# Optimization experiments

Hardware: AMD Instinct MI355X
Metric: run time of the kernel (lower is better)

Reference implementation:

```python
import jax, jax.numpy as jnp
import numpy as np

HIDDEN = 512
QK_DIM = HIDDEN // 8  # 64
B, H, W = 32, 32, 32


def conv1x1(x, w, b):
    # 1x1 conv == channel matmul: w [out_c, in_c], x [b, in_c, h, w]
    return jnp.einsum('oc,bchw->bohw', w, x) + b[None, :, None, None]


def setup_inputs() -> dict:
    key = jax.random.key(0)
    ks = jax.random.split(key, 10)
    s = 0.02
    return {
        'x': jax.random.normal(ks[0], (B, HIDDEN, H, W), jnp.float32),
        'pos_embedding': jax.random.normal(ks[1], (1, HIDDEN, 32, 32), jnp.float32),
        'query_w': jax.random.normal(ks[2], (QK_DIM, HIDDEN), jnp.float32) * s,
        'query_b': jax.random.normal(ks[3], (QK_DIM,), jnp.float32) * s,
        'key_w': jax.random.normal(ks[4], (QK_DIM, HIDDEN), jnp.float32) * s,
        'key_b': jax.random.normal(ks[5], (QK_DIM,), jnp.float32) * s,
        'value_w': jax.random.normal(ks[6], (HIDDEN, HIDDEN), jnp.float32) * s,
        'value_b': jax.random.normal(ks[7], (HIDDEN,), jnp.float32) * s,
        'out_w': jax.random.normal(ks[8], (HIDDEN, HIDDEN), jnp.float32) * s,
        'out_b': jax.random.normal(ks[9], (HIDDEN,), jnp.float32) * s,
    }


def reference(x, pos_embedding, query_w, query_b, key_w, key_b,
              value_w, value_b, out_w, out_b):
    b, c, h, w = x.shape
    n = h * w
    x = x + pos_embedding[:, :, :h, :w]
    q = conv1x1(x, query_w, query_b).reshape(b, -1, n)   # [b, d, n]
    k = conv1x1(x, key_w, key_b).reshape(b, -1, n)       # [b, d, n]
    v = conv1x1(x, value_w, value_b).reshape(b, -1, n)   # [b, c, n]
    # scores[b,i,j] = sum_d q[b,d,i] * k[b,d,j]  (no 1/sqrt(d) scaling, faithful)
    scores = jnp.einsum('bdi,bdj->bij', q, k)
    attn = jax.nn.softmax(scores, axis=-1)               # [b, n, n]
    # out[b,c,i] = sum_j v[b,c,j] * attn[b,i,j]
    out = jnp.einsum('bcj,bij->bci', v, attn).reshape(b, c, h, w)
    return conv1x1(out, out_w, out_b)
```

## Files before the change

kernel.cpp:

```cpp
#include <hip/hip_runtime.h>

#define BB 32
#define CC 512
#define DD 64
#define NN 1024
#define GRP 16
#define NGRP (BB / GRP)

typedef float4 f4;
typedef __attribute__((ext_vector_type(8))) short bf16x8;
typedef __attribute__((ext_vector_type(4))) float f32x4;
typedef __attribute__((ext_vector_type(4))) unsigned short us4;
typedef __attribute__((ext_vector_type(8))) unsigned short us8;

__device__ inline unsigned short bf16rn(float f) {
  union { float f; unsigned u; } v; v.f = f;
  unsigned r = v.u + 0x7fff + ((v.u >> 16) & 1);
  return (unsigned short)(r >> 16);
}

__device__ inline void gl_lds16(const void* g, void* l) {
  __builtin_amdgcn_global_load_lds(
      (const __attribute__((address_space(1))) unsigned int*)g,
      (__attribute__((address_space(3))) unsigned int*)l, 16, 0, 0);
}

__device__ inline void wait_vm0_barrier() {
  asm volatile("s_waitcnt vmcnt(0)" ::: "memory");
  __builtin_amdgcn_s_barrier();
}

__device__ inline int xcd_swz(int bid, int nwg) {
  return (bid & 7) * (nwg >> 3) + (bid >> 3);
}

template <int KDIM>
__device__ inline void gemm_core(const unsigned short* __restrict__ A,
                                 const unsigned short* __restrict__ Bt,
                                 int m0, int n0, int tid,
                                 unsigned short* sA, unsigned short* sB,
                                 f32x4 acc[4][4]) {
  const int wave = tid >> 6, lane = tid & 63;
  const int wm = (wave & 1) * 64, wn = (wave >> 1) * 64;
  const int fm = lane & 15;
  const int kq = lane >> 4;
  const int srow = lane >> 3;
  const int sg   = (lane & 7) ^ srow;

  const unsigned short* ga = A  + (size_t)(m0 + srow) * KDIM + sg * 8;
  const unsigned short* gb = Bt + (size_t)(n0 + srow) * KDIM + sg * 8;

  auto stage = [&](int buf, int k0) {
#pragma unroll
    for (int t = 0; t < 4; ++t) {
      const int R = wave * 32 + t * 8;
      gl_lds16(ga + (size_t)R * KDIM + k0, sA + buf * 8192 + R * 64);
      gl_lds16(gb + (size_t)R * KDIM + k0, sB + buf * 8192 + R * 64);
    }
  };

  stage(0, 0);
  wait_vm0_barrier();

  int cur = 0;
  for (int k0 = 0; k0 < KDIM; k0 += 64) {
    if (k0 + 64 < KDIM) stage(cur ^ 1, k0 + 64);
    const unsigned short* pA = sA + cur * 8192;
    const unsigned short* pB = sB + cur * 8192;
#pragma unroll
    for (int ks = 0; ks < 2; ++ks) {
      bf16x8 af[4], bfr[4];
#pragma unroll
      for (int i = 0; i < 4; ++i) {
        const int ra = wm + i * 16 + fm;
        const int rb = wn + i * 16 + fm;
        af[i]  = *(const bf16x8*)(pA + ra * 64 + ((ks * 4 + kq) ^ (ra & 7)) * 8);
        bfr[i] = *(const bf16x8*)(pB + rb * 64 + ((ks * 4 + kq) ^ (rb & 7)) * 8);
      }
#pragma unroll
      for (int i = 0; i < 4; ++i)
#pragma unroll
        for (int j = 0; j < 4; ++j)
          acc[i][j] = __builtin_amdgcn_mfma_f32_16x16x32_bf16(af[i], bfr[j], acc[i][j], 0, 0, 0);
    }
    wait_vm0_barrier();
    cur ^= 1;
  }
}

__global__ __launch_bounds__(256) void prep_w(
    const float* __restrict__ qw, const float* __restrict__ kw, const float* __restrict__ vw,
    const float* __restrict__ qb, const float* __restrict__ kb, const float* __restrict__ vb,
    const float* __restrict__ ow,
    unsigned short* __restrict__ wcat, unsigned short* __restrict__ owb,
    float* __restrict__ bcat) {
  int idx = blockIdx.x * 256 + threadIdx.x;
  if (idx < 640 * 512) {
    int row = idx >> 9;
    float v = (row < 64) ? qw[idx] : (row < 128) ? kw[idx - 64 * 512] : vw[idx - 128 * 512];
    wcat[idx] = bf16rn(v);
    if (idx < 640) bcat[idx] = (idx < 64) ? qb[idx] : (idx < 128) ? kb[idx - 64] : vb[idx - 128];
  } else {
    int j = idx - 640 * 512;
    owb[j] = bf16rn(ow[j]);
  }
}

__global__ __launch_bounds__(256) void prep_x(const float* __restrict__ x,
                                              const float* __restrict__ pos,
                                              unsigned short* __restrict__ A) {
  __shared__ float t[64][65];
  const int b = blockIdx.z, i0 = blockIdx.x * 64, c0 = blockIdx.y * 64;
  const int tid = threadIdx.x;
  const int ci = tid >> 4, il = (tid & 15) * 4;
  const float* xb = x + (size_t)b * CC * NN;
#pragma unroll
  for (int r = 0; r < 4; ++r) {
    int cl = r * 16 + ci;
    f4 xv = *(const f4*)(xb  + (size_t)(c0 + cl) * NN + i0 + il);
    f4 pv = *(const f4*)(pos + (size_t)(c0 + cl) * NN + i0 + il);
    t[cl][il + 0] = xv.x + pv.x;
    t[cl][il + 1] = xv.y + pv.y;
    t[cl][il + 2] = xv.z + pv.z;
    t[cl][il + 3] = xv.w + pv.w;
  }
  __syncthreads();
  const int iw = tid >> 2, cw = (tid & 3) * 16;
  unsigned short* dst = A + ((size_t)b * NN + i0 + iw) * CC + c0 + cw;
  us8 p0, p1;
#pragma unroll
  for (int j = 0; j < 8; ++j) p0[j] = bf16rn(t[cw + j][iw]);
#pragma unroll
  for (int j = 0; j < 8; ++j) p1[j] = bf16rn(t[cw + 8 + j][iw]);
  *(us8*)dst = p0;
  *(us8*)(dst + 8) = p1;
}

__global__ __launch_bounds__(256) void proj_gemm(
    const unsigned short* __restrict__ A, const unsigned short* __restrict__ wcat,
    const float* __restrict__ bcat,
    unsigned short* __restrict__ qo, unsigned short* __restrict__ ko,
    unsigned short* __restrict__ vto) {
  __shared__ unsigned short sA[16384], sB[16384];
  const int wid = xcd_swz(blockIdx.x, 1280);
  const int m0 = (wid & 7) * 128, n0 = ((wid >> 3) % 5) * 128, b = wid / 40;
  const int tid = threadIdx.x, wave = tid >> 6, lane = tid & 63;
  f32x4 acc[4][4];
#pragma unroll
  for (int i = 0; i < 4; ++i)
#pragma unroll
    for (int j = 0; j < 4; ++j) acc[i][j] = (f32x4)(0.0f);

  gemm_core<512>(A + (size_t)b * NN * CC, wcat, m0, n0, tid, sA, sB, acc);

  const int wm = (wave & 1) * 64, wn = (wave >> 1) * 64;
#pragma unroll
  for (int i = 0; i < 4; ++i)
#pragma unroll
    for (int j = 0; j < 4; ++j) {
      int col  = n0 + wn + j * 16 + (lane & 15);
      int rowb = m0 + wm + i * 16 + (lane >> 4) * 4;
      float bias = bcat[col];
      if (col < 64) {
#pragma unroll
        for (int r = 0; r < 4; ++r)
          qo[((size_t)b * NN + rowb + r) * DD + col] = bf16rn(acc[i][j][r] + bias);
      } else if (col < 128) {
#pragma unroll
        for (int r = 0; r < 4; ++r)
          ko[((size_t)b * NN + rowb + r) * DD + col - 64] = bf16rn(acc[i][j][r] + bias);
      } else {
        int c = col - 128;
        us4 pk;
#pragma unroll
        for (int r = 0; r < 4; ++r) pk[r] = bf16rn(acc[i][j][r] + bias);
        *(us4*)(vto + ((size_t)b * CC + c) * NN + rowb) = pk;
      }
    }
}

__global__ __launch_bounds__(256) void qkexp_kernel(
    const unsigned short* __restrict__ q, const unsigned short* __restrict__ k,
    float* __restrict__ lpart, unsigned short* __restrict__ P) {
  __shared__ unsigned short sQ[8192];
  __shared__ unsigned short sK[16384];
  __shared__ float wred[4][128];

  const int wid = xcd_swz(blockIdx.x, 8 * 2 * GRP);
  const int i0 = (wid & 7) * 128, jc = (wid >> 3) & 1, b = wid >> 4;
  const int jbase = jc * 512;
  const int tid = threadIdx.x, wave = tid >> 6, lane = tid & 63;
  const int wm = (wave & 1) * 64, wn = (wave >> 1) * 64;
  const int fm = lane & 15, kq = lane >> 4;
  const int srow = lane >> 3, sg = (lane & 7) ^ srow;

  const unsigned short* qb = q + (size_t)b * NN * DD;
  const unsigned short* kb = k + (size_t)b * NN * DD;

  auto stageK = [&](int buf, int j0) {
#pragma unroll
    for (int t = 0; t < 4; ++t) {
      const int R = wave * 32 + t * 8;
      gl_lds16(kb + (size_t)(j0 + R + srow) * DD + sg * 8, sK + buf * 8192 + R * 64);
    }
  };

#pragma unroll
  for (int t = 0; t < 4; ++t) {
    const int R = wave * 32 + t * 8;
    gl_lds16(qb + (size_t)(i0 + R + srow) * DD + sg * 8, sQ + R * 64);
  }
  stageK(0, jbase);
  wait_vm0_barrier();

  bf16x8 aq[4][2];
#pragma unroll
  for (int i = 0; i < 4; ++i)
#pragma unroll
    for (int kd = 0; kd < 2; ++kd) {
      const int ra = wm + i * 16 + fm;
      aq[i][kd] = *(const bf16x8*)(sQ + ra * 64 + ((kd * 4 + kq) ^ (ra & 7)) * 8);
    }

  float l_l[4] = {0.f, 0.f, 0.f, 0.f};

  int cur = 0;
#pragma unroll
  for (int jt = 0; jt < 4; ++jt) {
    if (jt < 3) stageK(cur ^ 1, jbase + (jt + 1) * 128);
    const unsigned short* pK = sK + cur * 8192;
    f32x4 S[4][4];
#pragma unroll
    for (int jk = 0; jk < 4; ++jk)
#pragma unroll
      for (int iq = 0; iq < 4; ++iq) S[jk][iq] = (f32x4)(0.0f);
#pragma unroll
    for (int kd = 0; kd < 2; ++kd) {
      bf16x8 bk[4];
#pragma unroll
      for (int jk = 0; jk < 4; ++jk) {
        const int rb = wn + jk * 16 + fm;
        bk[jk] = *(const bf16x8*)(pK + rb * 64 + ((kd * 4 + kq) ^ (rb & 7)) * 8);
      }
#pragma unroll
      for (int jk = 0; jk < 4; ++jk)
#pragma unroll
        for (int iq = 0; iq < 4; ++iq)
          S[jk][iq] = __builtin_amdgcn_mfma_f32_16x16x32_bf16(bk[jk], aq[iq][kd], S[jk][iq], 0, 0, 0);
    }
    us4 pk[4][4];
#pragma unroll
    for (int jk = 0; jk < 4; ++jk)
#pragma unroll
      for (int iq = 0; iq < 4; ++iq) {
#pragma unroll
        for (int r = 0; r < 4; ++r) {
          float e = __expf(S[jk][iq][r]);
          pk[jk][iq][r] = bf16rn(e);
          l_l[iq] += e;
        }
      }
    wait_vm0_barrier();
#pragma unroll
    for (int jk = 0; jk < 4; ++jk)
#pragma unroll
      for (int iq = 0; iq < 4; ++iq) {
        const int row = i0 + wm + iq * 16 + fm;
        const int col = jbase + jt * 128 + wn + jk * 16 + kq * 4;
        *(us4*)(P + ((size_t)b * NN + row) * NN + col) = pk[jk][iq];
      }
    cur ^= 1;
  }

#pragma unroll
  for (int iq = 0; iq < 4; ++iq) {
    float l = l_l[iq];
    l += __shfl_xor(l, 16, 64);
    l += __shfl_xor(l, 32, 64);
    l_l[iq] = l;
  }
  if (lane < 16) {
#pragma unroll
    for (int iq = 0; iq < 4; ++iq) wred[wave][wm + iq * 16 + fm] = l_l[iq];
  }
  __syncthreads();
  if (tid < 128) {
    const int a = tid >> 6;
    float l = wred[a][tid] + wred[a + 2][tid];
    lpart[((size_t)b * NN + i0 + tid) * 2 + jc] = l;
  }
}

__global__ __launch_bounds__(256) void pv_gemm(
    const unsigned short* __restrict__ P, const unsigned short* __restrict__ vT,
    const float* __restrict__ lpart, unsigned short* __restrict__ attnout) {
  __shared__ unsigned short sA[16384], sB[16384];
  const int wid = xcd_swz(blockIdx.x, 8 * 4 * GRP);
  const int m0 = (wid & 7) * 128, n0 = ((wid >> 3) & 3) * 128, b = wid >> 5;
  const int tid = threadIdx.x, wave = tid >> 6, lane = tid & 63;
  f32x4 acc[4][4];
#pragma unroll
  for (int i = 0; i < 4; ++i)
#pragma unroll
    for (int j = 0; j < 4; ++j) acc[i][j] = (f32x4)(0.0f);

  gemm_core<1024>(P + (size_t)b * NN * NN, vT + (size_t)b * CC * NN, m0, n0, tid, sA, sB, acc);

  const int wm = (wave & 1) * 64, wn = (wave >> 1) * 64;
  float inv[4][4];
#pragma unroll
  for (int i = 0; i < 4; ++i)
#pragma unroll
    for (int r = 0; r < 4; ++r) {
      const int row = m0 + wm + i * 16 + (lane >> 4) * 4 + r;
      float2 lp = *(const float2*)(lpart + ((size_t)b * NN + row) * 2);
      inv[i][r] = 1.0f / (lp.x + lp.y);
    }
#pragma unroll
  for (int i = 0; i < 4; ++i)
#pragma unroll
    for (int j = 0; j < 4; ++j) {
      int col  = n0 + wn + j * 16 + (lane & 15);
      int rowb = m0 + wm + i * 16 + (lane >> 4) * 4;
#pragma unroll
      for (int r = 0; r < 4; ++r)
        attnout[((size_t)b * NN + rowb + r) * CC + col] = bf16rn(acc[i][j][r] * inv[i][r]);
    }
}

__global__ __launch_bounds__(256) void outproj_gemm(
    const unsigned short* __restrict__ owb, const unsigned short* __restrict__ attnout,
    const float* __restrict__ ob, float* __restrict__ out) {
  __shared__ unsigned short sA[16384], sB[16384];
  const int wid = xcd_swz(blockIdx.x, 1024);
  const int m0 = (wid & 3) * 128, n0 = ((wid >> 2) & 7) * 128, b = wid >> 5;
  const int tid = threadIdx.x, wave = tid >> 6, lane = tid & 63;
  f32x4 acc[4][4];
#pragma unroll
  for (int i = 0; i < 4; ++i)
#pragma unroll
    for (int j = 0; j < 4; ++j) acc[i][j] = (f32x4)(0.0f);

  gemm_core<512>(owb, attnout + (size_t)b * NN * CC, m0, n0, tid, sA, sB, acc);

  const int wm = (wave & 1) * 64, wn = (wave >> 1) * 64;
#pragma unroll
  for (int i = 0; i < 4; ++i)
#pragma unroll
    for (int j = 0; j < 4; ++j) {
      int col  = n0 + wn + j * 16 + (lane & 15);
      int rowb = m0 + wm + i * 16 + (lane >> 4) * 4;
      f4 b4 = *(const f4*)(ob + rowb);
#pragma unroll
      for (int r = 0; r < 4; ++r)
        out[((size_t)b * CC + rowb + r) * NN + col] = acc[i][j][r] + ((const float*)&b4)[r];
    }
}

extern "C" void kernel_launch(void* const* d_in, const int* in_sizes, int n_in,
                              void* d_out, int out_size, void* d_ws, size_t ws_size,
                              hipStream_t stream) {
  const float* x   = (const float*)d_in[0];
  const float* pos = (const float*)d_in[1];
  const float* qw  = (const float*)d_in[2];
  const float* qb  = (const float*)d_in[3];
  const float* kw  = (const float*)d_in[4];
  const float* kb  = (const float*)d_in[5];
  const float* vw  = (const float*)d_in[6];
  const float* vb  = (const float*)d_in[7];
  const float* ow  = (const float*)d_in[8];
  const float* ob  = (const float*)d_in[9];
  float* out = (float*)d_out;

  char* w = (char*)d_ws;
  unsigned short* wcat = (unsigned short*)w; w += (size_t)640 * 512 * 2;
  unsigned short* owb  = (unsigned short*)w; w += (size_t)512 * 512 * 2;
  float*          bcat = (float*)w;          w += 640 * 4;
  unsigned short* A    = (unsigned short*)w; w += (size_t)BB * NN * CC * 2;
  unsigned short* q    = (unsigned short*)w; w += (size_t)BB * NN * DD * 2;
  unsigned short* k    = (unsigned short*)w; w += (size_t)BB * NN * DD * 2;
  unsigned short* vT   = (unsigned short*)w; w += (size_t)BB * CC * NN * 2;
  float*         lpart = (float*)w;          w += (size_t)BB * NN * 2 * 4;
  unsigned short* PG   = (unsigned short*)w; w += (size_t)GRP * NN * NN * 2;
  unsigned short* attnout = A;

  hipLaunchKernelGGL(prep_w, dim3(2304), dim3(256), 0, stream,
                     qw, kw, vw, qb, kb, vb, ow, wcat, owb, bcat);
  hipLaunchKernelGGL(prep_x, dim3(16, 8, 32), dim3(256), 0, stream, x, pos, A);
  hipLaunchKernelGGL(proj_gemm, dim3(1280), dim3(256), 0, stream,
                     A, wcat, bcat, q, k, vT);

  for (int g = 0; g < NGRP; ++g) {
    const unsigned short* qg  = q  + (size_t)g * GRP * NN * DD;
    const unsigned short* kg  = k  + (size_t)g * GRP * NN * DD;
    const unsigned short* vTg = vT + (size_t)g * GRP * CC * NN;
    float*                lpg = lpart + (size_t)g * GRP * NN * 2;
    unsigned short* aog = attnout + (size_t)g * GRP * NN * CC;
    hipLaunchKernelGGL(qkexp_kernel, dim3(8 * 2 * GRP), dim3(256), 0, stream,
                       qg, kg, lpg, PG);
    hipLaunchKernelGGL(pv_gemm, dim3(8 * 4 * GRP), dim3(256), 0, stream,
                       PG, vTg, lpg, aog);
  }

  hipLaunchKernelGGL(outproj_gemm, dim3(1024), dim3(256), 0, stream,
                     owb, attnout, ob, out);
}
```

Baseline: 283.5 us.

## Use triple-buffered BK=32 GEMM pipeline and defer P stores in scores kernel

The shared GEMM core moves from a double-buffered K-step of 64 with a full vmcnt(0) wait and barrier each step to a three-stage ring of 32-wide K tiles. Partial vmcnt waits let two tiles stay in flight, and the LDS footprint per block drops. The scores kernel now issues each P tile's global stores one iteration later, behind the next tile's MFMAs, and uses partial waits instead of draining all memory ops. The risks are finer-grained barriers with fewer MFMAs between them, and vmcnt counts that must exactly match the number of outstanding loads and stores.

After: 303.8 us. 7.2% more time.

```diff
diff --git a/kernel.cpp b/kernel.cpp
--- a/kernel.cpp
+++ b/kernel.cpp
@@ -35,56 +35,61 @@
 }
 
 template <int KDIM>
-__device__ inline void gemm_core(const unsigned short* __restrict__ A,
-                                 const unsigned short* __restrict__ Bt,
-                                 int m0, int n0, int tid,
-                                 unsigned short* sA, unsigned short* sB,
-                                 f32x4 acc[4][4]) {
+__device__ inline void gemm_core32(const unsigned short* __restrict__ A,
+                                   const unsigned short* __restrict__ Bt,
+                                   int m0, int n0, int tid,
+                                   unsigned short* sA, unsigned short* sB,
+                                   f32x4 acc[4][4]) {
+  constexpr int NT = KDIM / 32;
   const int wave = tid >> 6, lane = tid & 63;
   const int wm = (wave & 1) * 64, wn = (wave >> 1) * 64;
   const int fm = lane & 15;
   const int kq = lane >> 4;
-  const int srow = lane >> 3;
-  const int sg   = (lane & 7) ^ srow;
-
-  const unsigned short* ga = A  + (size_t)(m0 + srow) * KDIM + sg * 8;
-  const unsigned short* gb = Bt + (size_t)(n0 + srow) * KDIM + sg * 8;
+  const int srow = lane >> 2;
+  const int sg8  = ((lane & 3) ^ ((lane >> 3) & 3)) * 8;
+  const int slotA = (kq ^ ((fm >> 1) & 3)) * 8;
+
+  const unsigned short* ga = A  + (size_t)(m0 + srow) * KDIM + sg8;
+  const unsigned short* gb = Bt + (size_t)(n0 + srow) * KDIM + sg8;
 
   auto stage = [&](int buf, int k0) {
 #pragma unroll
-    for (int t = 0; t < 4; ++t) {
-      const int R = wave * 32 + t * 8;
-      gl_lds16(ga + (size_t)R * KDIM + k0, sA + buf * 8192 + R * 64);
-      gl_lds16(gb + (size_t)R * KDIM + k0, sB + buf * 8192 + R * 64);
+    for (int t = 0; t < 2; ++t) {
+      const int R0 = wave * 32 + t * 16;
+      gl_lds16(ga + (size_t)R0 * KDIM + k0, sA + buf * 4096 + R0 * 32);
+      gl_lds16(gb + (size_t)R0 * KDIM + k0, sB + buf * 4096 + R0 * 32);
     }
   };
 
   stage(0, 0);
-  wait_vm0_barrier();
+  stage(1, 32);
 
   int cur = 0;
-  for (int k0 = 0; k0 < KDIM; k0 += 64) {
-    if (k0 + 64 < KDIM) stage(cur ^ 1, k0 + 64);
-    const unsigned short* pA = sA + cur * 8192;
-    const unsigned short* pB = sB + cur * 8192;
-#pragma unroll
-    for (int ks = 0; ks < 2; ++ks) {
-      bf16x8 af[4], bfr[4];
-#pragma unroll
-      for (int i = 0; i < 4; ++i) {
-        const int ra = wm + i * 16 + fm;
-        const int rb = wn + i * 16 + fm;
-        af[i]  = *(const bf16x8*)(pA + ra * 64 + ((ks * 4 + kq) ^ (ra & 7)) * 8);
-        bfr[i] = *(const bf16x8*)(pB + rb * 64 + ((ks * 4 + kq) ^ (rb & 7)) * 8);
-      }
-#pragma unroll
-      for (int i = 0; i < 4; ++i)
-#pragma unroll
-        for (int j = 0; j < 4; ++j)
-          acc[i][j] = __builtin_amdgcn_mfma_f32_16x16x32_bf16(af[i], bfr[j], acc[i][j], 0, 0, 0);
-    }
-    wait_vm0_barrier();
-    cur ^= 1;
+  for (int i = 0; i < NT; ++i) {
+    if (i + 1 < NT) {
+      asm volatile("s_waitcnt vmcnt(4)" ::: "memory");
+    } else {
+      asm volatile("s_waitcnt vmcnt(0)" ::: "memory");
+    }
+    __builtin_amdgcn_s_barrier();
+    if (i + 2 < NT) {
+      int nb = cur + 2; if (nb >= 3) nb -= 3;
+      stage(nb, (i + 2) * 32);
+    }
+    const unsigned short* pA = sA + cur * 4096;
+    const unsigned short* pB = sB + cur * 4096;
+    bf16x8 af[4], bfr[4];
+#pragma unroll
+    for (int ii = 0; ii < 4; ++ii) {
+      af[ii]  = *(const bf16x8*)(pA + (wm + ii * 16 + fm) * 32 + slotA);
+      bfr[ii] = *(const bf16x8*)(pB + (wn + ii * 16 + fm) * 32 + slotA);
+    }
+#pragma unroll
+    for (int ii = 0; ii < 4; ++ii)
+#pragma unroll
+      for (int j = 0; j < 4; ++j)
+        acc[ii][j] = __builtin_amdgcn_mfma_f32_16x16x32_bf16(af[ii], bfr[j], acc[ii][j], 0, 0, 0);
+    cur += 1; if (cur >= 3) cur -= 3;
   }
 }
 
@@ -141,7 +146,7 @@
     const float* __restrict__ bcat,
     unsigned short* __restrict__ qo, unsigned short* __restrict__ ko,
     unsigned short* __restrict__ vto) {
-  __shared__ unsigned short sA[16384], sB[16384];
+  __shared__ unsigned short sA[12288], sB[12288];
   const int wid = xcd_swz(blockIdx.x, 1280);
   const int m0 = (wid & 7) * 128, n0 = ((wid >> 3) % 5) * 128, b = wid / 40;
   const int tid = threadIdx.x, wave = tid >> 6, lane = tid & 63;
@@ -151,7 +156,7 @@
 #pragma unroll
     for (int j = 0; j < 4; ++j) acc[i][j] = (f32x4)(0.0f);
 
-  gemm_core<512>(A + (size_t)b * NN * CC, wcat, m0, n0, tid, sA, sB, acc);
+  gemm_core32<512>(A + (size_t)b * NN * CC, wcat, m0, n0, tid, sA, sB, acc);
 
   const int wm = (wave & 1) * 64, wn = (wave >> 1) * 64;
 #pragma unroll
@@ -223,11 +228,23 @@
     }
 
   float l_l[4] = {0.f, 0.f, 0.f, 0.f};
+  us4 pk[4][4];
+  int pjt = 0;
 
   int cur = 0;
 #pragma unroll
   for (int jt = 0; jt < 4; ++jt) {
     if (jt < 3) stageK(cur ^ 1, jbase + (jt + 1) * 128);
+    if (jt > 0) {
+#pragma unroll
+      for (int jk = 0; jk < 4; ++jk)
+#pragma unroll
+        for (int iq = 0; iq < 4; ++iq) {
+          const int row = i0 + wm + iq * 16 + fm;
+          const int col = jbase + pjt * 128 + wn + jk * 16 + kq * 4;
+          *(us4*)(P + ((size_t)b * NN + row) * NN + col) = pk[jk][iq];
+        }
+    }
     const unsigned short* pK = sK + cur * 8192;
     f32x4 S[4][4];
 #pragma unroll
@@ -248,7 +265,6 @@
         for (int iq = 0; iq < 4; ++iq)
           S[jk][iq] = __builtin_amdgcn_mfma_f32_16x16x32_bf16(bk[jk], aq[iq][kd], S[jk][iq], 0, 0, 0);
     }
-    us4 pk[4][4];
 #pragma unroll
     for (int jk = 0; jk < 4; ++jk)
 #pragma unroll
@@ -260,17 +276,22 @@
           l_l[iq] += e;
         }
       }
-    wait_vm0_barrier();
-#pragma unroll
-    for (int jk = 0; jk < 4; ++jk)
-#pragma unroll
-      for (int iq = 0; iq < 4; ++iq) {
-        const int row = i0 + wm + iq * 16 + fm;
-        const int col = jbase + jt * 128 + wn + jk * 16 + kq * 4;
-        *(us4*)(P + ((size_t)b * NN + row) * NN + col) = pk[jk][iq];
-      }
+    pjt = jt;
+    if (jt < 3) {
+      if (jt == 0) { asm volatile("s_waitcnt vmcnt(0)" ::: "memory"); }
+      else         { asm volatile("s_waitcnt vmcnt(16)" ::: "memory"); }
+      __builtin_amdgcn_s_barrier();
+    }
     cur ^= 1;
   }
+#pragma unroll
+  for (int jk = 0; jk < 4; ++jk)
+#pragma unroll
+    for (int iq = 0; iq < 4; ++iq) {
+      const int row = i0 + wm + iq * 16 + fm;
+      const int col = jbase + 3 * 128 + wn + jk * 16 + kq * 4;
+      *(us4*)(P + ((size_t)b * NN + row) * NN + col) = pk[jk][iq];
+    }
 
 #pragma unroll
   for (int iq = 0; iq < 4; ++iq) {
@@ -294,7 +315,7 @@
 __global__ __launch_bounds__(256) void pv_gemm(
     const unsigned short* __restrict__ P, const unsigned short* __restrict__ vT,
     const float* __restrict__ lpart, unsigned short* __restrict__ attnout) {
-  __shared__ unsigned short sA[16384], sB[16384];
+  __shared__ unsigned short sA[12288], sB[12288];
   const int wid = xcd_swz(blockIdx.x, 8 * 4 * GRP);
   const int m0 = (wid & 7) * 128, n0 = ((wid >> 3) & 3) * 128, b = wid >> 5;
   const int tid = threadIdx.x, wave = tid >> 6, lane = tid & 63;
@@ -304,7 +325,7 @@
 #pragma unroll
     for (int j = 0; j < 4; ++j) acc[i][j] = (f32x4)(0.0f);
 
-  gemm_core<1024>(P + (size_t)b * NN * NN, vT + (size_t)b * CC * NN, m0, n0, tid, sA, sB, acc);
+  gemm_core32<1024>(P + (size_t)b * NN * NN, vT + (size_t)b * CC * NN, m0, n0, tid, sA, sB, acc);
 
   const int wm = (wave & 1) * 64, wn = (wave >> 1) * 64;
   float inv[4][4];
@@ -331,7 +352,7 @@
 __global__ __launch_bounds__(256) void outproj_gemm(
     const unsigned short* __restrict__ owb, const unsigned short* __restrict__ attnout,
     const float* __restrict__ ob, float* __restrict__ out) {
-  __shared__ unsigned short sA[16384], sB[16384];
+  __shared__ unsigned short sA[12288], sB[12288];
   const int wid = xcd_swz(blockIdx.x, 1024);
   const int m0 = (wid & 3) * 128, n0 = ((wid >> 2) & 7) * 128, b = wid >> 5;
   const int tid = threadIdx.x, wave = tid >> 6, lane = tid & 63;
@@ -341,7 +362,7 @@
 #pragma unroll
     for (int j = 0; j < 4; ++j) acc[i][j] = (f32x4)(0.0f);
 
-  gemm_core<512>(owb, attnout + (size_t)b * NN * CC, m0, n0, tid, sA, sB, acc);
+  gemm_core32<512>(owb, attnout + (size_t)b * NN * CC, m0, n0, tid, sA, sB, acc);
 
   const int wm = (wave & 1) * 64, wn = (wave >> 1) * 64;
 #pragma unroll
```

## Rewrite output projection GEMM with 256x256 tiles and double-buffered LDS pipeline

Applied to the files above, without the earlier changes.

Replaces the 128x128-tile output projection (1024 blocks of 256 threads) with a 256x256-tile kernel using 8 waves per block (256 blocks of 512 threads). Global-to-LDS loads go into double-buffered, XOR-swizzled shared memory and are staged in pieces interleaved with the MFMA phases, with explicit vmcnt waits and barriers. The aim is more operand reuse per LDS load and overlap of loads with compute. The cost is 128 KB of LDS and a large accumulator per wave, which limits the GPU to one block per CU, and 256 blocks may underfill the device.

New measurement: 288.2 us. Within noise of the previous version (+1.7%).

```diff
diff --git a/kernel.cpp b/kernel.cpp
--- a/kernel.cpp
+++ b/kernel.cpp
@@ -328,32 +328,97 @@
     }
 }
 
-__global__ __launch_bounds__(256) void outproj_gemm(
+__global__ __launch_bounds__(512, 1) void outproj_gemm8(
     const unsigned short* __restrict__ owb, const unsigned short* __restrict__ attnout,
     const float* __restrict__ ob, float* __restrict__ out) {
-  __shared__ unsigned short sA[16384], sB[16384];
-  const int wid = xcd_swz(blockIdx.x, 1024);
-  const int m0 = (wid & 3) * 128, n0 = ((wid >> 2) & 7) * 128, b = wid >> 5;
+  __shared__ unsigned short sA[2][16384];
+  __shared__ unsigned short sB[2][16384];
+
+  const int wid = xcd_swz(blockIdx.x, 256);
+  const int m0 = (wid & 1) * 256, n0 = ((wid >> 1) & 3) * 256, b = wid >> 3;
   const int tid = threadIdx.x, wave = tid >> 6, lane = tid & 63;
-  f32x4 acc[4][4];
-#pragma unroll
-  for (int i = 0; i < 4; ++i)
+  const int wave_m = wave >> 2, wave_n = wave & 3;
+  const int wm = wave_m * 128, wn = wave_n * 64;
+  const int fm = lane & 15, kq = lane >> 4;
+  const int srow = lane >> 3, sg = (lane & 7) ^ srow;
+
+  const unsigned short* ga = owb + (size_t)(m0 + srow) * 512 + sg * 8;
+  const unsigned short* gb = attnout + (size_t)b * NN * CC + (size_t)(n0 + srow) * 512 + sg * 8;
+
+  auto stageB4 = [&](int buf, int k0) {
+#pragma unroll
+    for (int s = 0; s < 4; ++s) {
+      const int R = s * 64 + wave * 8;
+      gl_lds16(gb + (size_t)R * 512 + k0, &sB[buf][R * 64]);
+    }
+  };
+  auto stageA2 = [&](int buf, int k0, int h) {
+#pragma unroll
+    for (int t = 0; t < 2; ++t) {
+      const int R = (h + t * 2) * 64 + wave * 8;
+      gl_lds16(ga + (size_t)R * 512 + k0, &sA[buf][R * 64]);
+    }
+  };
+
+  f32x4 acc[8][4];
+#pragma unroll
+  for (int i = 0; i < 8; ++i)
 #pragma unroll
     for (int j = 0; j < 4; ++j) acc[i][j] = (f32x4)(0.0f);
 
-  gemm_core<512>(owb, attnout + (size_t)b * NN * CC, m0, n0, tid, sA, sB, acc);
-
-  const int wm = (wave & 1) * 64, wn = (wave >> 1) * 64;
-#pragma unroll
-  for (int i = 0; i < 4; ++i)
+  stageB4(0, 0); stageA2(0, 0, 0); stageA2(0, 0, 1);
+
+  for (int t = 0; t < 8; ++t) {
+    const int cur = t & 1;
+    const int k0n = (t + 1) * 64;
+    const unsigned short* pA = sA[cur];
+    const unsigned short* pB = sB[cur];
+
+#pragma unroll
+    for (int p = 0; p < 4; ++p) {
+      const int ih = p >> 1, kw = p & 1;
+      if (p == 0) {
+        asm volatile("s_waitcnt vmcnt(2)" ::: "memory");
+        __builtin_amdgcn_s_barrier();
+        if (t < 7) stageB4(cur ^ 1, k0n);
+      } else if (p == 2) {
+        if (t < 7) { asm volatile("s_waitcnt vmcnt(6)" ::: "memory"); }
+        else       { asm volatile("s_waitcnt vmcnt(0)" ::: "memory"); }
+        __builtin_amdgcn_s_barrier();
+        if (t < 7) stageA2(cur ^ 1, k0n, 1);
+      } else if (p == 1) {
+        if (t < 7) stageA2(cur ^ 1, k0n, 0);
+      }
+      bf16x8 af[4], bfr[4];
+#pragma unroll
+      for (int i = 0; i < 4; ++i) {
+        const int ra = wm + ih * 64 + i * 16 + fm;
+        af[i] = *(const bf16x8*)(pA + ra * 64 + ((kw * 4 + kq) ^ (ra & 7)) * 8);
+      }
+#pragma unroll
+      for (int j = 0; j < 4; ++j) {
+        const int rb = wn + j * 16 + fm;
+        bfr[j] = *(const bf16x8*)(pB + rb * 64 + ((kw * 4 + kq) ^ (rb & 7)) * 8);
+      }
+#pragma unroll
+      for (int i = 0; i < 4; ++i)
+#pragma unroll
+        for (int j = 0; j < 4; ++j)
+          acc[ih * 4 + i][j] =
+              __builtin_amdgcn_mfma_f32_16x16x32_bf16(af[i], bfr[j], acc[ih * 4 + i][j], 0, 0, 0);
+    }
+  }
+
+#pragma unroll
+  for (int ig = 0; ig < 8; ++ig)
 #pragma unroll
     for (int j = 0; j < 4; ++j) {
-      int col  = n0 + wn + j * 16 + (lane & 15);
-      int rowb = m0 + wm + i * 16 + (lane >> 4) * 4;
+      int col  = n0 + wn + j * 16 + fm;
+      int rowb = m0 + wm + ig * 16 + kq * 4;
       f4 b4 = *(const f4*)(ob + rowb);
 #pragma unroll
       for (int r = 0; r < 4; ++r)
-        out[((size_t)b * CC + rowb + r) * NN + col] = acc[i][j][r] + ((const float*)&b4)[r];
+        out[((size_t)b * CC + rowb + r) * NN + col] = acc[ig][j][r] + ((const float*)&b4)[r];
     }
 }
 
@@ -402,6 +467,6 @@
                        PG, vTg, lpg, aog);
   }
 
-  hipLaunchKernelGGL(outproj_gemm, dim3(1024), dim3(256), 0, stream,
+  hipLaunchKernelGGL(outproj_gemm8, dim3(256), dim3(512), 0, stream,
                      owb, attnout, ob, out);
 }
```
